# Performance work log

Hardware: AMD Instinct MI355X
Metric: run time of the kernel (lower is better)

The kernel has to match this reference:

```python
import jax, jax.numpy as jnp
import numpy as np

D_MODEL = 1024
N_HEADS = 16
DEPTH = D_MODEL // N_HEADS
B, S = 2, 2048


def setup_inputs() -> dict:
    key = jax.random.key(0)
    ks = jax.random.split(key, 11)
    scale = 1.0 / np.sqrt(D_MODEL)
    return {
        "q": jax.random.normal(ks[0], (B, S, D_MODEL), jnp.float32),
        "k": jax.random.normal(ks[1], (B, S, D_MODEL), jnp.float32),
        "v": jax.random.normal(ks[2], (B, S, D_MODEL), jnp.float32),
        "wq": jax.random.normal(ks[3], (D_MODEL, D_MODEL), jnp.float32) * scale,
        "bq": jnp.zeros((D_MODEL,), jnp.float32),
        "wk": jax.random.normal(ks[4], (D_MODEL, D_MODEL), jnp.float32) * scale,
        "bk": jnp.zeros((D_MODEL,), jnp.float32),
        "wv": jax.random.normal(ks[5], (D_MODEL, D_MODEL), jnp.float32) * scale,
        "bv": jnp.zeros((D_MODEL,), jnp.float32),
        "wo": jax.random.normal(ks[6], (D_MODEL, D_MODEL), jnp.float32) * scale,
        "bo": jnp.zeros((D_MODEL,), jnp.float32),
    }


def _mha(q, k, v, wq, bq, wk, bk, wv, bv, wo, bo):
    b, s, _ = q.shape
    # separate QKV projections
    qh = (q @ wq + bq).reshape(b, s, N_HEADS, DEPTH).transpose(0, 2, 1, 3)  # [b,h,s,d]
    kh = (k @ wk + bk).reshape(b, s, N_HEADS, DEPTH).transpose(0, 2, 1, 3)
    vh = (v @ wv + bv).reshape(b, s, N_HEADS, DEPTH).transpose(0, 2, 1, 3)
    # keras.layers.Attention default: UNSCALED dot-product scores, causal mask
    scores = jnp.einsum("bhqd,bhkd->bhqk", qh, kh)  # [b,h,s,s]
    causal = jnp.tril(jnp.ones((s, s), bool))
    scores = jnp.where(causal, scores, jnp.float32(-1e9))
    attn = jax.nn.softmax(scores, axis=-1)
    out = jnp.einsum("bhqk,bhkd->bhqd", attn, vh)  # [b,h,s,d]
    out = out.transpose(0, 2, 1, 3).reshape(b, s, D_MODEL)
    return out @ wo + bo


def reference(q, k, v, wq, bq, wk, bk, wv, bv, wo, bo):
    return _mha(q, k, v, wq, bq, wk, bk, wv, bv, wo, bo)
```

## Files before the change

kernel.cpp:

```cpp
#include <hip/hip_runtime.h>
#include <stdint.h>

#define AS1q __attribute__((address_space(1)))
#define AS3q __attribute__((address_space(3)))

typedef unsigned short US;
typedef __bf16 bf16x8 __attribute__((ext_vector_type(8)));
typedef float f32x4 __attribute__((ext_vector_type(4)));
typedef float f32x2 __attribute__((ext_vector_type(2)));
typedef __bf16 bf16x2 __attribute__((ext_vector_type(2)));

__device__ __forceinline__ US f2bf(float f) {
  union { float f; uint32_t u; } c; c.f = f;
  uint32_t u = c.u;
  return (US)((u + 0x7fffu + ((u >> 16) & 1u)) >> 16);
}

__device__ __forceinline__ bf16x8 asb(uint4 u) {
  union { uint4 u; bf16x8 b; } c; c.u = u; return c.b;
}

__device__ __forceinline__ void gload16(const void* g, void* l) {
  __builtin_amdgcn_global_load_lds((AS1q void*)(void*)g, (AS3q void*)l, 16, 0, 0);
}

__global__ void prep_kernel(const float* __restrict__ q, const float* __restrict__ k,
                            const float* __restrict__ v,
                            const float* __restrict__ w0, const float* __restrict__ w1,
                            const float* __restrict__ w2, const float* __restrict__ w3,
                            US* __restrict__ qb, US* __restrict__ kb, US* __restrict__ vb,
                            US* __restrict__ t0, US* __restrict__ t1,
                            US* __restrict__ t2, US* __restrict__ t3) {
  __shared__ US T[64 * 68];
  const int bx = blockIdx.x;
  const int t = threadIdx.x;
  if (bx < 6144) {
    const int ten = bx >> 11, chunk = bx & 2047;
    const float* s; US* d;
    if (ten == 0)      { s = q; d = qb; }
    else if (ten == 1) { s = k; d = kb; }
    else               { s = v; d = vb; }
    int i = (chunk * 256 + t) * 8;
    float4 f0 = *(const float4*)&s[i];
    float4 f1 = *(const float4*)&s[i + 4];
    ushort4 u0, u1;
    u0.x = f2bf(f0.x); u0.y = f2bf(f0.y); u0.z = f2bf(f0.z); u0.w = f2bf(f0.w);
    u1.x = f2bf(f1.x); u1.y = f2bf(f1.y); u1.z = f2bf(f1.z); u1.w = f2bf(f1.w);
    *(ushort4*)&d[i] = u0;
    *(ushort4*)&d[i + 4] = u1;
    return;
  }
  const int idx = bx - 6144;
  const int wsel = idx >> 8, rem = idx & 255;
  const int n0 = (rem & 15) * 64, k0 = (rem >> 4) * 64;
  const float* W; US* Wt;
  if (wsel == 0)      { W = w0; Wt = t0; }
  else if (wsel == 1) { W = w1; Wt = t1; }
  else if (wsel == 2) { W = w2; Wt = t2; }
  else                { W = w3; Wt = t3; }
#pragma unroll
  for (int it = 0; it < 4; ++it) {
    int p = t + it * 256;
    int row = p >> 4, c4 = (p & 15) * 4;
    float4 f = *(const float4*)&W[(k0 + row) * 1024 + n0 + c4];
    ushort4 u;
    u.x = f2bf(f.x); u.y = f2bf(f.y); u.z = f2bf(f.z); u.w = f2bf(f.w);
    *(ushort4*)&T[row * 68 + c4] = u;
  }
  __syncthreads();
#pragma unroll
  for (int it = 0; it < 4; ++it) {
    int p = t + it * 256;
    int rn = p >> 4, ck = (p & 15) * 4;
    ushort4 o;
    o.x = T[(ck + 0) * 68 + rn];
    o.y = T[(ck + 1) * 68 + rn];
    o.z = T[(ck + 2) * 68 + rn];
    o.w = T[(ck + 3) * 68 + rn];
    *(ushort4*)&Wt[(n0 + rn) * 1024 + k0 + ck] = o;
  }
}

template <bool SWAP>
__device__ __forceinline__ void gemm_core(const US* A, const US* Wt,
                                          int m0, int n0, US* As, US* Bs,
                                          f32x4 acc[4][4]) {
  const int tid = threadIdx.x;
  const int wave = tid >> 6, lane = tid & 63;
  const int quad = lane >> 4, l16 = lane & 15;
  const int wm = wave >> 1, wn = wave & 1;
#pragma unroll
  for (int i = 0; i < 4; ++i)
#pragma unroll
    for (int j = 0; j < 4; ++j) acc[i][j] = (f32x4)0.0f;
  const int p = wave * 64 + lane;
  const int arow0 = p >> 2, koff = (p & 3) * 8;
  for (int k0 = 0; k0 < 1024; k0 += 32) {
    gload16(A + (m0 + arow0) * 1024 + k0 + koff, As + wave * 512);
    gload16(A + (m0 + arow0 + 64) * 1024 + k0 + koff, As + 2048 + wave * 512);
    gload16(Wt + (n0 + arow0) * 1024 + k0 + koff, Bs + wave * 512);
    gload16(Wt + (n0 + arow0 + 64) * 1024 + k0 + koff, Bs + 2048 + wave * 512);
    __syncthreads();
    uint4 af[4], bf_[4];
#pragma unroll
    for (int mt = 0; mt < 4; ++mt)
      af[mt] = *(const uint4*)&As[(wm * 64 + mt * 16 + l16) * 32 + quad * 8];
#pragma unroll
    for (int nt = 0; nt < 4; ++nt)
      bf_[nt] = *(const uint4*)&Bs[(wn * 64 + nt * 16 + l16) * 32 + quad * 8];
#pragma unroll
    for (int i = 0; i < 4; ++i)
#pragma unroll
      for (int j = 0; j < 4; ++j) {
        if (SWAP)
          acc[i][j] = __builtin_amdgcn_mfma_f32_16x16x32_bf16(asb(bf_[i]), asb(af[j]),
                                                              acc[i][j], 0, 0, 0);
        else
          acc[i][j] = __builtin_amdgcn_mfma_f32_16x16x32_bf16(asb(af[i]), asb(bf_[j]),
                                                              acc[i][j], 0, 0, 0);
      }
    __syncthreads();
  }
}

__global__ __launch_bounds__(256, 4) void gemm_qkv_kernel(
    const US* __restrict__ qb, const US* __restrict__ kb, const US* __restrict__ vb,
    const US* __restrict__ wfT,
    const float* __restrict__ bq, const float* __restrict__ bk, const float* __restrict__ bv,
    US* __restrict__ qh, US* __restrict__ kh, US* __restrict__ vt) {
  __shared__ __align__(16) US As[4096], Bs[4096];
  const int m0 = blockIdx.x * 128, n0 = blockIdx.y * 128;
  const int which = n0 >> 10;
  const int nl0 = n0 & 1023;
  const US* A = (which == 0) ? qb : (which == 1) ? kb : vb;
  const float* bias = (which == 0) ? bq : (which == 1) ? bk : bv;
  const int tid = threadIdx.x, wave = tid >> 6, lane = tid & 63;
  const int quad = lane >> 4, l16 = lane & 15;
  const int wm = wave >> 1, wn = wave & 1;
  f32x4 acc[4][4];
  if (which == 2) {
    gemm_core<true>(A, wfT, m0, n0, As, Bs, acc);
#pragma unroll
    for (int nt = 0; nt < 4; ++nt) {
      int dg = nl0 + wn * 64 + nt * 16 + quad * 4;
#pragma unroll
      for (int r = 0; r < 4; ++r) {
        int d = dg + r;
        float bval = bias[d];
        int hh = d >> 6, dd = d & 63;
#pragma unroll
        for (int mt = 0; mt < 4; ++mt) {
          int sg = m0 + wm * 64 + mt * 16;
          int bb = sg >> 11, ss = sg & 2047;
          vt[(((size_t)bb * 16 + hh) * 64 + dd) * 2048 + ss + l16] =
              f2bf(acc[nt][mt][r] + bval);
        }
      }
    }
  } else {
    gemm_core<false>(A, wfT, m0, n0, As, Bs, acc);
    US* O = (which == 0) ? qh : kh;
#pragma unroll
    for (int nt = 0; nt < 4; ++nt) {
      int nl = nl0 + wn * 64 + nt * 16 + l16;
      float bval = bias[nl];
      int hh = nl >> 6, d = nl & 63;
#pragma unroll
      for (int mt = 0; mt < 4; ++mt) {
#pragma unroll
        for (int r = 0; r < 4; ++r) {
          int m = m0 + wm * 64 + mt * 16 + quad * 4 + r;
          int bb = m >> 11, s = m & 2047;
          O[((bb * 16 + hh) * 2048 + s) * 64 + d] = f2bf(acc[mt][nt][r] + bval);
        }
      }
    }
  }
}

__global__ __launch_bounds__(256, 4) void gemm_out_kernel(
    const US* __restrict__ ao, const US* __restrict__ woT,
    const float* __restrict__ bo, float* __restrict__ out) {
  __shared__ __align__(16) US As[4096], Bs[2048];
  const int m0 = blockIdx.x * 128, n0 = blockIdx.y * 64;
  const int tid = threadIdx.x;
  const int wave = tid >> 6, lane = tid & 63;
  const int quad = lane >> 4, l16 = lane & 15;
  f32x4 acc[2][4];
#pragma unroll
  for (int i = 0; i < 2; ++i)
#pragma unroll
    for (int j = 0; j < 4; ++j) acc[i][j] = (f32x4)0.0f;
  const int arow0 = tid >> 2, koff = (tid & 3) * 8;
  for (int k0 = 0; k0 < 1024; k0 += 32) {
    gload16(ao + (m0 + arow0) * 1024 + k0 + koff, As + wave * 512);
    gload16(ao + (m0 + arow0 + 64) * 1024 + k0 + koff, As + 2048 + wave * 512);
    gload16(woT + (n0 + arow0) * 1024 + k0 + koff, Bs + wave * 512);
    __syncthreads();
    uint4 af[2], bf_[4];
#pragma unroll
    for (int mt = 0; mt < 2; ++mt)
      af[mt] = *(const uint4*)&As[(wave * 32 + mt * 16 + l16) * 32 + quad * 8];
#pragma unroll
    for (int nt = 0; nt < 4; ++nt)
      bf_[nt] = *(const uint4*)&Bs[(nt * 16 + l16) * 32 + quad * 8];
#pragma unroll
    for (int mt = 0; mt < 2; ++mt)
#pragma unroll
      for (int nt = 0; nt < 4; ++nt)
        acc[mt][nt] = __builtin_amdgcn_mfma_f32_16x16x32_bf16(asb(af[mt]), asb(bf_[nt]),
                                                              acc[mt][nt], 0, 0, 0);
    __syncthreads();
  }
#pragma unroll
  for (int nt = 0; nt < 4; ++nt) {
    int n = n0 + nt * 16 + l16;
    float bval = bo[n];
#pragma unroll
    for (int mt = 0; mt < 2; ++mt) {
#pragma unroll
      for (int r = 0; r < 4; ++r) {
        int m = m0 + wave * 32 + mt * 16 + quad * 4 + r;
        out[m * 1024 + n] = acc[mt][nt][r] + bval;
      }
    }
  }
}

__global__ __launch_bounds__(512, 6) void attn_kernel(
    const US* __restrict__ qh, const US* __restrict__ kh,
    const US* __restrict__ vt, US* __restrict__ aout) {
  __shared__ __align__(16) US Ks[2][4096];
  __shared__ __align__(16) US Vs[2][4096];
  __shared__ __align__(16) union UU {
    struct { US Qs[4096]; US Ps[8 * 640]; } s;
    struct { float Oex[4][16][65]; float lEx[4][16]; } e;
  } u;
  const int tid = threadIdx.x;
  const int wave = tid >> 6, lane = tid & 63;
  const int quad = lane >> 4, l16 = lane & 15;
  const int w_m = wave & 3, w_k = wave >> 2;
  const int bh = blockIdx.x;
  const int b = bh >> 4, h = bh & 15;
  const int g = blockIdx.y;

  int t0, t1;
  if (g < 11)      { t0 = 31 - g; t1 = -1; }
  else if (g < 19) { int j = g - 11; t0 = 16 - j; t1 = j; }
  else if (g < 23) { t0 = 17 + (g - 19); t1 = -1; }
  else             { t0 = 8; t1 = -1; }

  const int srow = tid >> 3, sc = (tid & 7) ^ (srow & 7);
  const US* gkb = kh + (size_t)bh * 2048 * 64;
  const US* gvb = vt + (size_t)bh * 64 * 2048;

  for (int ei = 0; ei < 2; ++ei) {
    const int qt = ei ? t1 : t0;
    if (qt < 0) break;
    const int q0 = qt * 64;
    __syncthreads();
    {
      const US* gq = qh + ((size_t)bh * 2048 + q0) * 64;
      gload16(gq + srow * 64 + sc * 8, u.s.Qs + wave * 512);
      gload16(gkb + srow * 64 + sc * 8, Ks[0] + wave * 512);
      gload16(gvb + srow * 2048 + sc * 8, Vs[0] + wave * 512);
    }
    __syncthreads();

    const int qrow = w_m * 16 + l16;
    uint4 aq0 = *(const uint4*)&u.s.Qs[qrow * 64 + ((quad ^ (qrow & 7)) * 8)];
    uint4 aq1 = *(const uint4*)&u.s.Qs[qrow * 64 + (((4 + quad) ^ (qrow & 7)) * 8)];

    float l_part[4] = {0.f, 0.f, 0.f, 0.f};
    f32x4 Of[4];
#pragma unroll
    for (int nt = 0; nt < 4; ++nt) Of[nt] = (f32x4)0.0f;
    const int grow_base = q0 + w_m * 16 + quad * 4;

    US* pw = u.s.Ps + wave * 640;

    for (int kt = 0; kt <= qt; ++kt) {
      const int cb = kt & 1;
      if (kt) __syncthreads();
      if (kt < qt) {
        const US* gk = gkb + (kt + 1) * 64 * 64;
        const US* gv = gvb + (kt + 1) * 64;
        gload16(gk + srow * 64 + sc * 8, Ks[cb ^ 1] + wave * 512);
        gload16(gv + srow * 2048 + sc * 8, Vs[cb ^ 1] + wave * 512);
      }
      const US* Kc = Ks[cb];
      const US* Vc = Vs[cb];

      f32x4 sacc[2];
      sacc[0] = (f32x4)0.0f; sacc[1] = (f32x4)0.0f;
#pragma unroll
      for (int nt = 0; nt < 2; ++nt) {
        int krow = w_k * 32 + nt * 16 + l16;
        uint4 bk0 = *(const uint4*)&Kc[krow * 64 + ((quad ^ (krow & 7)) * 8)];
        sacc[nt] = __builtin_amdgcn_mfma_f32_16x16x32_bf16(asb(aq0), asb(bk0), sacc[nt], 0, 0, 0);
      }
#pragma unroll
      for (int nt = 0; nt < 2; ++nt) {
        int krow = w_k * 32 + nt * 16 + l16;
        uint4 bk1 = *(const uint4*)&Kc[krow * 64 + (((4 + quad) ^ (krow & 7)) * 8)];
        sacc[nt] = __builtin_amdgcn_mfma_f32_16x16x32_bf16(asb(aq1), asb(bk1), sacc[nt], 0, 0, 0);
      }
      if (kt == qt) {
#pragma unroll
        for (int nt = 0; nt < 2; ++nt) {
          int gcol = q0 + w_k * 32 + nt * 16 + l16;
#pragma unroll
          for (int r = 0; r < 4; ++r)
            if (gcol > grow_base + r) sacc[nt][r] = -1e30f;
        }
      }

#pragma unroll
      for (int nt = 0; nt < 2; ++nt) {
#pragma unroll
        for (int r = 0; r < 4; r += 2) {
          float e0 = __expf(sacc[nt][r]);
          float e1 = __expf(sacc[nt][r + 1]);
          l_part[r] += e0;
          l_part[r + 1] += e1;
          f32x2 fv; fv[0] = e0; fv[1] = e1;
          bf16x2 bv2 = __builtin_convertvector(fv, bf16x2);
          union { bf16x2 b; ushort2 u; } cc; cc.b = bv2;
          pw[(quad * 4 + r) * 40 + nt * 16 + l16] = cc.u.x;
          pw[(quad * 4 + r + 1) * 40 + nt * 16 + l16] = cc.u.y;
        }
      }
      __asm__ volatile("s_waitcnt lgkmcnt(0)" ::: "memory");

      uint4 ap = *(const uint4*)&pw[l16 * 40 + quad * 8];
#pragma unroll
      for (int nt = 0; nt < 4; ++nt) {
        int vrow = nt * 16 + l16;
        uint4 bv_ = *(const uint4*)&Vc[vrow * 64 + (((w_k * 4 + quad) ^ (vrow & 7)) * 8)];
        Of[nt] = __builtin_amdgcn_mfma_f32_16x16x32_bf16(asb(ap), asb(bv_), Of[nt], 0, 0, 0);
      }
    }

    float l_red[4];
#pragma unroll
    for (int r = 0; r < 4; ++r) {
      float s = l_part[r];
#pragma unroll
      for (int off = 1; off < 16; off <<= 1) s += __shfl_xor(s, off, 64);
      l_red[r] = s;
    }

    __syncthreads();
    if (w_k == 1) {
#pragma unroll
      for (int nt = 0; nt < 4; ++nt)
#pragma unroll
        for (int r = 0; r < 4; ++r)
          u.e.Oex[w_m][quad * 4 + r][nt * 16 + l16] = Of[nt][r];
      if (l16 == 0) {
#pragma unroll
        for (int r = 0; r < 4; ++r) u.e.lEx[w_m][quad * 4 + r] = l_red[r];
      }
    }
    __syncthreads();
    if (w_k == 0) {
#pragma unroll
      for (int r = 0; r < 4; ++r) {
        float ltot = l_red[r] + u.e.lEx[w_m][quad * 4 + r];
        float inv = 1.0f / ltot;
        int row = grow_base + r;
#pragma unroll
        for (int nt = 0; nt < 4; ++nt) {
          float o = Of[nt][r] + u.e.Oex[w_m][quad * 4 + r][nt * 16 + l16];
          aout[((size_t)b * 2048 + row) * 1024 + h * 64 + nt * 16 + l16] = f2bf(o * inv);
        }
      }
    }
  }
}

extern "C" void kernel_launch(void* const* d_in, const int* in_sizes, int n_in,
                              void* d_out, int out_size, void* d_ws, size_t ws_size,
                              hipStream_t stream) {
  const float* q  = (const float*)d_in[0];
  const float* k  = (const float*)d_in[1];
  const float* v  = (const float*)d_in[2];
  const float* wq = (const float*)d_in[3];
  const float* bq = (const float*)d_in[4];
  const float* wk = (const float*)d_in[5];
  const float* bk = (const float*)d_in[6];
  const float* wv = (const float*)d_in[7];
  const float* bv = (const float*)d_in[8];
  const float* wo = (const float*)d_in[9];
  const float* bo = (const float*)d_in[10];
  float* out = (float*)d_out;

  char* ws = (char*)d_ws;
  const size_t MB = 1024 * 1024;
  US* qb  = (US*)(ws + 0 * MB);
  US* kb  = (US*)(ws + 8 * MB);
  US* vb  = (US*)(ws + 16 * MB);
  US* wqT = (US*)(ws + 24 * MB);
  US* wkT = (US*)(ws + 26 * MB);
  US* wvT = (US*)(ws + 28 * MB);
  US* woT = (US*)(ws + 30 * MB);
  US* qh  = (US*)(ws + 32 * MB);
  US* kh  = (US*)(ws + 40 * MB);
  US* vt  = (US*)(ws + 48 * MB);
  US* ao  = (US*)(ws + 56 * MB);

  prep_kernel<<<7168, 256, 0, stream>>>(q, k, v, wq, wk, wv, wo,
                                        qb, kb, vb, wqT, wkT, wvT, woT);
  gemm_qkv_kernel<<<dim3(32, 24), 256, 0, stream>>>(qb, kb, vb, wqT,
                                                    bq, bk, bv, qh, kh, vt);
  attn_kernel<<<dim3(32, 24), 512, 0, stream>>>(qh, kh, vt, ao);
  gemm_out_kernel<<<dim3(32, 16), 256, 0, stream>>>(ao, woT, bo, out);
}
```

Measured before the change: 208.6 us.

## Use 32x32x16 MFMA in attention with 4 waves and exp2-prescaled Q

The attention kernel moves from 8 waves using 16x16x32 MFMA tiles to 4 waves per block using 32x32x16 MFMA tiles. Each wave now owns a 32x32 score tile, which cuts LDS fragment reloads per flop and the number of MFMA issues. Q is prescaled by log2(e) in the QKV projection epilogue so the softmax can call the native exp2 in place of __expf. The trade-offs are half as many waves per block, more registers per wave, and wider cross-lane reductions of the row sums.

```diff
diff --git a/kernel.cpp b/kernel.cpp
--- a/kernel.cpp
+++ b/kernel.cpp
@@ -7,8 +7,11 @@
 typedef unsigned short US;
 typedef __bf16 bf16x8 __attribute__((ext_vector_type(8)));
 typedef float f32x4 __attribute__((ext_vector_type(4)));
+typedef float f32x16 __attribute__((ext_vector_type(16)));
 typedef float f32x2 __attribute__((ext_vector_type(2)));
 typedef __bf16 bf16x2 __attribute__((ext_vector_type(2)));
+
+#define LOG2E 1.44269504088896340736f
 
 __device__ __forceinline__ US f2bf(float f) {
   union { float f; uint32_t u; } c; c.f = f;
@@ -160,6 +163,7 @@
   } else {
     gemm_core<false>(A, wfT, m0, n0, As, Bs, acc);
     US* O = (which == 0) ? qh : kh;
+    const float scale = (which == 0) ? LOG2E : 1.0f;
 #pragma unroll
     for (int nt = 0; nt < 4; ++nt) {
       int nl = nl0 + wn * 64 + nt * 16 + l16;
@@ -171,7 +175,7 @@
         for (int r = 0; r < 4; ++r) {
           int m = m0 + wm * 64 + mt * 16 + quad * 4 + r;
           int bb = m >> 11, s = m & 2047;
-          O[((bb * 16 + hh) * 2048 + s) * 64 + d] = f2bf(acc[mt][nt][r] + bval);
+          O[((bb * 16 + hh) * 2048 + s) * 64 + d] = f2bf((acc[mt][nt][r] + bval) * scale);
         }
       }
     }
@@ -227,19 +231,19 @@
   }
 }
 
-__global__ __launch_bounds__(512, 6) void attn_kernel(
+__global__ __launch_bounds__(256, 3) void attn_kernel(
     const US* __restrict__ qh, const US* __restrict__ kh,
     const US* __restrict__ vt, US* __restrict__ aout) {
   __shared__ __align__(16) US Ks[2][4096];
   __shared__ __align__(16) US Vs[2][4096];
   __shared__ __align__(16) union UU {
-    struct { US Qs[4096]; US Ps[8 * 640]; } s;
-    struct { float Oex[4][16][65]; float lEx[4][16]; } e;
+    struct { US Qs[4096]; US Ps[4][1280]; } s;
+    struct { float Oex[64][65]; float lEx[64]; } e;
   } u;
   const int tid = threadIdx.x;
   const int wave = tid >> 6, lane = tid & 63;
-  const int quad = lane >> 4, l16 = lane & 15;
-  const int w_m = wave & 3, w_k = wave >> 2;
+  const int l31 = lane & 31, lh = lane >> 5;
+  const int w_m = wave & 1, w_k = wave >> 1;
   const int bh = blockIdx.x;
   const int b = bh >> 4, h = bh & 15;
   const int g = blockIdx.y;
@@ -250,7 +254,10 @@
   else if (g < 23) { t0 = 17 + (g - 19); t1 = -1; }
   else             { t0 = 8; t1 = -1; }
 
-  const int srow = tid >> 3, sc = (tid & 7) ^ (srow & 7);
+  const int p1 = tid, p2 = tid + 256;
+  const int row1 = p1 >> 3, c1 = (p1 & 7) ^ (row1 & 7);
+  const int row2 = p2 >> 3, c2 = (p2 & 7) ^ (row2 & 7);
+
   const US* gkb = kh + (size_t)bh * 2048 * 64;
   const US* gvb = vt + (size_t)bh * 64 * 2048;
 
@@ -261,23 +268,28 @@
     __syncthreads();
     {
       const US* gq = qh + ((size_t)bh * 2048 + q0) * 64;
-      gload16(gq + srow * 64 + sc * 8, u.s.Qs + wave * 512);
-      gload16(gkb + srow * 64 + sc * 8, Ks[0] + wave * 512);
-      gload16(gvb + srow * 2048 + sc * 8, Vs[0] + wave * 512);
-    }
-    __syncthreads();
-
-    const int qrow = w_m * 16 + l16;
-    uint4 aq0 = *(const uint4*)&u.s.Qs[qrow * 64 + ((quad ^ (qrow & 7)) * 8)];
-    uint4 aq1 = *(const uint4*)&u.s.Qs[qrow * 64 + (((4 + quad) ^ (qrow & 7)) * 8)];
-
-    float l_part[4] = {0.f, 0.f, 0.f, 0.f};
-    f32x4 Of[4];
-#pragma unroll
-    for (int nt = 0; nt < 4; ++nt) Of[nt] = (f32x4)0.0f;
-    const int grow_base = q0 + w_m * 16 + quad * 4;
-
-    US* pw = u.s.Ps + wave * 640;
+      gload16(gq + row1 * 64 + c1 * 8, u.s.Qs + wave * 512);
+      gload16(gq + row2 * 64 + c2 * 8, u.s.Qs + 2048 + wave * 512);
+      gload16(gkb + row1 * 64 + c1 * 8, Ks[0] + wave * 512);
+      gload16(gkb + row2 * 64 + c2 * 8, Ks[0] + 2048 + wave * 512);
+      gload16(gvb + row1 * 2048 + c1 * 8, Vs[0] + wave * 512);
+      gload16(gvb + row2 * 2048 + c2 * 8, Vs[0] + 2048 + wave * 512);
+    }
+    __syncthreads();
+
+    const int ql = w_m * 32 + l31;
+    uint4 aq[4];
+#pragma unroll
+    for (int dc = 0; dc < 4; ++dc)
+      aq[dc] = *(const uint4*)&u.s.Qs[ql * 64 + (((dc * 2 + lh) ^ (ql & 7)) * 8)];
+
+    float l_part[16];
+#pragma unroll
+    for (int r = 0; r < 16; ++r) l_part[r] = 0.0f;
+    f32x16 Of0 = (f32x16)0.0f, Of1 = (f32x16)0.0f;
+
+    US* pw = u.s.Ps[wave];
+    const int kl = w_k * 32 + l31;
 
     for (int kt = 0; kt <= qt; ++kt) {
       const int cb = kt & 1;
@@ -285,95 +297,92 @@
       if (kt < qt) {
         const US* gk = gkb + (kt + 1) * 64 * 64;
         const US* gv = gvb + (kt + 1) * 64;
-        gload16(gk + srow * 64 + sc * 8, Ks[cb ^ 1] + wave * 512);
-        gload16(gv + srow * 2048 + sc * 8, Vs[cb ^ 1] + wave * 512);
+        gload16(gk + row1 * 64 + c1 * 8, Ks[cb ^ 1] + wave * 512);
+        gload16(gk + row2 * 64 + c2 * 8, Ks[cb ^ 1] + 2048 + wave * 512);
+        gload16(gv + row1 * 2048 + c1 * 8, Vs[cb ^ 1] + wave * 512);
+        gload16(gv + row2 * 2048 + c2 * 8, Vs[cb ^ 1] + 2048 + wave * 512);
       }
       const US* Kc = Ks[cb];
       const US* Vc = Vs[cb];
 
-      f32x4 sacc[2];
-      sacc[0] = (f32x4)0.0f; sacc[1] = (f32x4)0.0f;
-#pragma unroll
-      for (int nt = 0; nt < 2; ++nt) {
-        int krow = w_k * 32 + nt * 16 + l16;
-        uint4 bk0 = *(const uint4*)&Kc[krow * 64 + ((quad ^ (krow & 7)) * 8)];
-        sacc[nt] = __builtin_amdgcn_mfma_f32_16x16x32_bf16(asb(aq0), asb(bk0), sacc[nt], 0, 0, 0);
-      }
-#pragma unroll
-      for (int nt = 0; nt < 2; ++nt) {
-        int krow = w_k * 32 + nt * 16 + l16;
-        uint4 bk1 = *(const uint4*)&Kc[krow * 64 + (((4 + quad) ^ (krow & 7)) * 8)];
-        sacc[nt] = __builtin_amdgcn_mfma_f32_16x16x32_bf16(asb(aq1), asb(bk1), sacc[nt], 0, 0, 0);
+      f32x16 sacc = (f32x16)0.0f;
+#pragma unroll
+      for (int dc = 0; dc < 4; ++dc) {
+        uint4 kb_ = *(const uint4*)&Kc[kl * 64 + (((dc * 2 + lh) ^ (kl & 7)) * 8)];
+        sacc = __builtin_amdgcn_mfma_f32_32x32x16_bf16(asb(aq[dc]), asb(kb_), sacc, 0, 0, 0);
       }
       if (kt == qt) {
-#pragma unroll
-        for (int nt = 0; nt < 2; ++nt) {
-          int gcol = q0 + w_k * 32 + nt * 16 + l16;
-#pragma unroll
-          for (int r = 0; r < 4; ++r)
-            if (gcol > grow_base + r) sacc[nt][r] = -1e30f;
+        int gcol = q0 + w_k * 32 + l31;
+#pragma unroll
+        for (int r = 0; r < 16; ++r) {
+          int grow = q0 + w_m * 32 + 4 * lh + 8 * (r >> 2) + (r & 3);
+          if (gcol > grow) sacc[r] = -1e30f;
         }
       }
 
 #pragma unroll
-      for (int nt = 0; nt < 2; ++nt) {
-#pragma unroll
-        for (int r = 0; r < 4; r += 2) {
-          float e0 = __expf(sacc[nt][r]);
-          float e1 = __expf(sacc[nt][r + 1]);
-          l_part[r] += e0;
-          l_part[r + 1] += e1;
-          f32x2 fv; fv[0] = e0; fv[1] = e1;
-          bf16x2 bv2 = __builtin_convertvector(fv, bf16x2);
-          union { bf16x2 b; ushort2 u; } cc; cc.b = bv2;
-          pw[(quad * 4 + r) * 40 + nt * 16 + l16] = cc.u.x;
-          pw[(quad * 4 + r + 1) * 40 + nt * 16 + l16] = cc.u.y;
+      for (int r = 0; r < 16; r += 2) {
+        float e0 = __builtin_amdgcn_exp2f(sacc[r]);
+        float e1 = __builtin_amdgcn_exp2f(sacc[r + 1]);
+        l_part[r] += e0;
+        l_part[r + 1] += e1;
+        f32x2 fv; fv[0] = e0; fv[1] = e1;
+        bf16x2 bv2 = __builtin_convertvector(fv, bf16x2);
+        union { bf16x2 b; ushort2 u; } cc; cc.b = bv2;
+        int row0 = 4 * lh + 8 * (r >> 2) + (r & 3);
+        pw[row0 * 40 + l31] = cc.u.x;
+        pw[(row0 + 1) * 40 + l31] = cc.u.y;
+      }
+      __asm__ volatile("s_waitcnt lgkmcnt(0)" ::: "memory");
+
+      uint4 ap0 = *(const uint4*)&pw[l31 * 40 + lh * 8];
+      uint4 ap1 = *(const uint4*)&pw[l31 * 40 + 16 + lh * 8];
+#pragma unroll
+      for (int dh = 0; dh < 2; ++dh) {
+        int vrow = dh * 32 + l31;
+        uint4 bv0 = *(const uint4*)&Vc[vrow * 64 + (((w_k * 4 + lh) ^ (vrow & 7)) * 8)];
+        uint4 bv1 = *(const uint4*)&Vc[vrow * 64 + (((w_k * 4 + 2 + lh) ^ (vrow & 7)) * 8)];
+        if (dh == 0) {
+          Of0 = __builtin_amdgcn_mfma_f32_32x32x16_bf16(asb(ap0), asb(bv0), Of0, 0, 0, 0);
+          Of0 = __builtin_amdgcn_mfma_f32_32x32x16_bf16(asb(ap1), asb(bv1), Of0, 0, 0, 0);
+        } else {
+          Of1 = __builtin_amdgcn_mfma_f32_32x32x16_bf16(asb(ap0), asb(bv0), Of1, 0, 0, 0);
+          Of1 = __builtin_amdgcn_mfma_f32_32x32x16_bf16(asb(ap1), asb(bv1), Of1, 0, 0, 0);
         }
       }
-      __asm__ volatile("s_waitcnt lgkmcnt(0)" ::: "memory");
-
-      uint4 ap = *(const uint4*)&pw[l16 * 40 + quad * 8];
-#pragma unroll
-      for (int nt = 0; nt < 4; ++nt) {
-        int vrow = nt * 16 + l16;
-        uint4 bv_ = *(const uint4*)&Vc[vrow * 64 + (((w_k * 4 + quad) ^ (vrow & 7)) * 8)];
-        Of[nt] = __builtin_amdgcn_mfma_f32_16x16x32_bf16(asb(ap), asb(bv_), Of[nt], 0, 0, 0);
-      }
-    }
-
-    float l_red[4];
-#pragma unroll
-    for (int r = 0; r < 4; ++r) {
-      float s = l_part[r];
-#pragma unroll
-      for (int off = 1; off < 16; off <<= 1) s += __shfl_xor(s, off, 64);
-      l_red[r] = s;
+    }
+
+#pragma unroll
+    for (int r = 0; r < 16; ++r) {
+#pragma unroll
+      for (int off = 1; off < 32; off <<= 1)
+        l_part[r] += __shfl_xor(l_part[r], off, 64);
     }
 
     __syncthreads();
     if (w_k == 1) {
 #pragma unroll
-      for (int nt = 0; nt < 4; ++nt)
-#pragma unroll
-        for (int r = 0; r < 4; ++r)
-          u.e.Oex[w_m][quad * 4 + r][nt * 16 + l16] = Of[nt][r];
-      if (l16 == 0) {
-#pragma unroll
-        for (int r = 0; r < 4; ++r) u.e.lEx[w_m][quad * 4 + r] = l_red[r];
+      for (int r = 0; r < 16; ++r) {
+        int row = w_m * 32 + 4 * lh + 8 * (r >> 2) + (r & 3);
+        u.e.Oex[row][l31] = Of0[r];
+        u.e.Oex[row][32 + l31] = Of1[r];
+        if (l31 == 0) u.e.lEx[row] = l_part[r];
       }
     }
     __syncthreads();
     if (w_k == 0) {
 #pragma unroll
-      for (int r = 0; r < 4; ++r) {
-        float ltot = l_red[r] + u.e.lEx[w_m][quad * 4 + r];
+      for (int r = 0; r < 16; ++r) {
+        int rl = 4 * lh + 8 * (r >> 2) + (r & 3);
+        int row = w_m * 32 + rl;
+        float ltot = l_part[r] + u.e.lEx[row];
         float inv = 1.0f / ltot;
-        int row = grow_base + r;
-#pragma unroll
-        for (int nt = 0; nt < 4; ++nt) {
-          float o = Of[nt][r] + u.e.Oex[w_m][quad * 4 + r][nt * 16 + l16];
-          aout[((size_t)b * 2048 + row) * 1024 + h * 64 + nt * 16 + l16] = f2bf(o * inv);
-        }
+        int grow = q0 + row;
+        float o0 = Of0[r] + u.e.Oex[row][l31];
+        float o1 = Of1[r] + u.e.Oex[row][32 + l31];
+        US* dst = aout + ((size_t)b * 2048 + grow) * 1024 + h * 64;
+        dst[l31] = f2bf(o0 * inv);
+        dst[32 + l31] = f2bf(o1 * inv);
       }
     }
   }
@@ -413,6 +422,6 @@
                                         qb, kb, vb, wqT, wkT, wvT, woT);
   gemm_qkv_kernel<<<dim3(32, 24), 256, 0, stream>>>(qb, kb, vb, wqT,
                                                     bq, bk, bv, qh, kh, vt);
-  attn_kernel<<<dim3(32, 24), 512, 0, stream>>>(qh, kh, vt, ao);
+  attn_kernel<<<dim3(32, 24), 256, 0, stream>>>(qh, kh, vt, ao);
   gemm_out_kernel<<<dim3(32, 16), 256, 0, stream>>>(ao, woT, bo, out);
 }
```

Result: no change. 208.9 us (+0.2%).

## Restructure causal attention around 32x32 MFMA, 128-key tiles and register-resident P

Applied to the files above, without the earlier changes.

Rewrites the attention kernel to use 256-thread blocks with 32x32x16 bf16 MFMAs over 128-key tiles. It computes S transposed so the exp'd probabilities are repacked into MFMA operands through cross-lane shuffles instead of a round trip through LDS. log2(e) is folded into the Q projection epilogue so softmax uses the native exp2. Each block handles a balanced pair of query tiles (qt, 31-qt) on a 32x16 grid, and the final normalization writes 16-byte vector stores. The cost is more LDS per block (72 KB) and lower occupancy, and the 128-key diagonal tile wastes some masked work.

```diff
diff --git a/kernel.cpp b/kernel.cpp
--- a/kernel.cpp
+++ b/kernel.cpp
@@ -7,8 +7,11 @@
 typedef unsigned short US;
 typedef __bf16 bf16x8 __attribute__((ext_vector_type(8)));
 typedef float f32x4 __attribute__((ext_vector_type(4)));
+typedef float f32x16 __attribute__((ext_vector_type(16)));
 typedef float f32x2 __attribute__((ext_vector_type(2)));
 typedef __bf16 bf16x2 __attribute__((ext_vector_type(2)));
+
+#define LOG2E 1.44269504088896340736f
 
 __device__ __forceinline__ US f2bf(float f) {
   union { float f; uint32_t u; } c; c.f = f;
@@ -18,6 +21,12 @@
 
 __device__ __forceinline__ bf16x8 asb(uint4 u) {
   union { uint4 u; bf16x8 b; } c; c.u = u; return c.b;
+}
+
+__device__ __forceinline__ uint32_t pk2(float a, float b) {
+  f32x2 fv; fv[0] = a; fv[1] = b;
+  bf16x2 bb = __builtin_convertvector(fv, bf16x2);
+  union { bf16x2 b; uint32_t u; } c; c.b = bb; return c.u;
 }
 
 __device__ __forceinline__ void gload16(const void* g, void* l) {
@@ -160,6 +169,7 @@
   } else {
     gemm_core<false>(A, wfT, m0, n0, As, Bs, acc);
     US* O = (which == 0) ? qh : kh;
+    const float scale = (which == 0) ? LOG2E : 1.0f;
 #pragma unroll
     for (int nt = 0; nt < 4; ++nt) {
       int nl = nl0 + wn * 64 + nt * 16 + l16;
@@ -171,7 +181,7 @@
         for (int r = 0; r < 4; ++r) {
           int m = m0 + wm * 64 + mt * 16 + quad * 4 + r;
           int bb = m >> 11, s = m & 2047;
-          O[((bb * 16 + hh) * 2048 + s) * 64 + d] = f2bf(acc[mt][nt][r] + bval);
+          O[((bb * 16 + hh) * 2048 + s) * 64 + d] = f2bf((acc[mt][nt][r] + bval) * scale);
         }
       }
     }
@@ -227,154 +237,178 @@
   }
 }
 
-__global__ __launch_bounds__(512, 6) void attn_kernel(
+__global__ __launch_bounds__(256, 2) void attn_kernel(
     const US* __restrict__ qh, const US* __restrict__ kh,
     const US* __restrict__ vt, US* __restrict__ aout) {
-  __shared__ __align__(16) US Ks[2][4096];
-  __shared__ __align__(16) US Vs[2][4096];
-  __shared__ __align__(16) union UU {
-    struct { US Qs[4096]; US Ps[8 * 640]; } s;
-    struct { float Oex[4][16][65]; float lEx[4][16]; } e;
-  } u;
+  __shared__ __align__(16) char arena[73728];
+  US* KsA = (US*)arena;
+  US* VsA = (US*)(arena + 32768);
+  US* Qs  = (US*)(arena + 65536);
+  float* Oex = (float*)arena;
+  float* lEx = (float*)(arena + 34816);
+
   const int tid = threadIdx.x;
   const int wave = tid >> 6, lane = tid & 63;
-  const int quad = lane >> 4, l16 = lane & 15;
-  const int w_m = wave & 3, w_k = wave >> 2;
+  const int l31 = lane & 31, lh = lane >> 5;
+  const int w_m = wave & 1, w_k = wave >> 1;
   const int bh = blockIdx.x;
   const int b = bh >> 4, h = bh & 15;
-  const int g = blockIdx.y;
-
-  int t0, t1;
-  if (g < 11)      { t0 = 31 - g; t1 = -1; }
-  else if (g < 19) { int j = g - 11; t0 = 16 - j; t1 = j; }
-  else if (g < 23) { t0 = 17 + (g - 19); t1 = -1; }
-  else             { t0 = 8; t1 = -1; }
-
-  const int srow = tid >> 3, sc = (tid & 7) ^ (srow & 7);
+  const int jg = blockIdx.y;
+
   const US* gkb = kh + (size_t)bh * 2048 * 64;
   const US* gvb = vt + (size_t)bh * 64 * 2048;
 
   for (int ei = 0; ei < 2; ++ei) {
-    const int qt = ei ? t1 : t0;
-    if (qt < 0) break;
+    const int qt = ei ? jg : (31 - jg);
     const int q0 = qt * 64;
+    const int nit = (qt >> 1) + 1;
     __syncthreads();
     {
       const US* gq = qh + ((size_t)bh * 2048 + q0) * 64;
-      gload16(gq + srow * 64 + sc * 8, u.s.Qs + wave * 512);
-      gload16(gkb + srow * 64 + sc * 8, Ks[0] + wave * 512);
-      gload16(gvb + srow * 2048 + sc * 8, Vs[0] + wave * 512);
-    }
-    __syncthreads();
-
-    const int qrow = w_m * 16 + l16;
-    uint4 aq0 = *(const uint4*)&u.s.Qs[qrow * 64 + ((quad ^ (qrow & 7)) * 8)];
-    uint4 aq1 = *(const uint4*)&u.s.Qs[qrow * 64 + (((4 + quad) ^ (qrow & 7)) * 8)];
-
-    float l_part[4] = {0.f, 0.f, 0.f, 0.f};
-    f32x4 Of[4];
-#pragma unroll
-    for (int nt = 0; nt < 4; ++nt) Of[nt] = (f32x4)0.0f;
-    const int grow_base = q0 + w_m * 16 + quad * 4;
-
-    US* pw = u.s.Ps + wave * 640;
-
-    for (int kt = 0; kt <= qt; ++kt) {
-      const int cb = kt & 1;
-      if (kt) __syncthreads();
-      if (kt < qt) {
-        const US* gk = gkb + (kt + 1) * 64 * 64;
-        const US* gv = gvb + (kt + 1) * 64;
-        gload16(gk + srow * 64 + sc * 8, Ks[cb ^ 1] + wave * 512);
-        gload16(gv + srow * 2048 + sc * 8, Vs[cb ^ 1] + wave * 512);
-      }
-      const US* Kc = Ks[cb];
-      const US* Vc = Vs[cb];
-
-      f32x4 sacc[2];
-      sacc[0] = (f32x4)0.0f; sacc[1] = (f32x4)0.0f;
-#pragma unroll
-      for (int nt = 0; nt < 2; ++nt) {
-        int krow = w_k * 32 + nt * 16 + l16;
-        uint4 bk0 = *(const uint4*)&Kc[krow * 64 + ((quad ^ (krow & 7)) * 8)];
-        sacc[nt] = __builtin_amdgcn_mfma_f32_16x16x32_bf16(asb(aq0), asb(bk0), sacc[nt], 0, 0, 0);
-      }
-#pragma unroll
-      for (int nt = 0; nt < 2; ++nt) {
-        int krow = w_k * 32 + nt * 16 + l16;
-        uint4 bk1 = *(const uint4*)&Kc[krow * 64 + (((4 + quad) ^ (krow & 7)) * 8)];
-        sacc[nt] = __builtin_amdgcn_mfma_f32_16x16x32_bf16(asb(aq1), asb(bk1), sacc[nt], 0, 0, 0);
-      }
-      if (kt == qt) {
-#pragma unroll
-        for (int nt = 0; nt < 2; ++nt) {
-          int gcol = q0 + w_k * 32 + nt * 16 + l16;
-#pragma unroll
-          for (int r = 0; r < 4; ++r)
-            if (gcol > grow_base + r) sacc[nt][r] = -1e30f;
-        }
-      }
-
-#pragma unroll
-      for (int nt = 0; nt < 2; ++nt) {
-#pragma unroll
-        for (int r = 0; r < 4; r += 2) {
-          float e0 = __expf(sacc[nt][r]);
-          float e1 = __expf(sacc[nt][r + 1]);
-          l_part[r] += e0;
-          l_part[r + 1] += e1;
-          f32x2 fv; fv[0] = e0; fv[1] = e1;
-          bf16x2 bv2 = __builtin_convertvector(fv, bf16x2);
-          union { bf16x2 b; ushort2 u; } cc; cc.b = bv2;
-          pw[(quad * 4 + r) * 40 + nt * 16 + l16] = cc.u.x;
-          pw[(quad * 4 + r + 1) * 40 + nt * 16 + l16] = cc.u.y;
-        }
-      }
-      __asm__ volatile("s_waitcnt lgkmcnt(0)" ::: "memory");
-
-      uint4 ap = *(const uint4*)&pw[l16 * 40 + quad * 8];
-#pragma unroll
-      for (int nt = 0; nt < 4; ++nt) {
-        int vrow = nt * 16 + l16;
-        uint4 bv_ = *(const uint4*)&Vc[vrow * 64 + (((w_k * 4 + quad) ^ (vrow & 7)) * 8)];
-        Of[nt] = __builtin_amdgcn_mfma_f32_16x16x32_bf16(asb(ap), asb(bv_), Of[nt], 0, 0, 0);
-      }
-    }
-
-    float l_red[4];
-#pragma unroll
-    for (int r = 0; r < 4; ++r) {
-      float s = l_part[r];
-#pragma unroll
-      for (int off = 1; off < 16; off <<= 1) s += __shfl_xor(s, off, 64);
-      l_red[r] = s;
-    }
-
-    __syncthreads();
-    if (w_k == 1) {
-#pragma unroll
-      for (int nt = 0; nt < 4; ++nt)
-#pragma unroll
-        for (int r = 0; r < 4; ++r)
-          u.e.Oex[w_m][quad * 4 + r][nt * 16 + l16] = Of[nt][r];
-      if (l16 == 0) {
-#pragma unroll
-        for (int r = 0; r < 4; ++r) u.e.lEx[w_m][quad * 4 + r] = l_red[r];
-      }
-    }
-    __syncthreads();
-    if (w_k == 0) {
-#pragma unroll
-      for (int r = 0; r < 4; ++r) {
-        float ltot = l_red[r] + u.e.lEx[w_m][quad * 4 + r];
-        float inv = 1.0f / ltot;
-        int row = grow_base + r;
-#pragma unroll
-        for (int nt = 0; nt < 4; ++nt) {
-          float o = Of[nt][r] + u.e.Oex[w_m][quad * 4 + r][nt * 16 + l16];
-          aout[((size_t)b * 2048 + row) * 1024 + h * 64 + nt * 16 + l16] = f2bf(o * inv);
-        }
-      }
+#pragma unroll
+      for (int ro = 0; ro < 2; ++ro) {
+        int p = tid + ro * 256;
+        int row = p >> 3, c = (p & 7) ^ (row & 7);
+        gload16(gq + row * 64 + c * 8, Qs + ro * 2048 + wave * 512);
+      }
+#pragma unroll
+      for (int ro = 0; ro < 4; ++ro) {
+        int p = tid + ro * 256;
+        int row = p >> 3, c = (p & 7) ^ (row & 7);
+        gload16(gkb + row * 64 + c * 8, KsA + ro * 2048 + wave * 512);
+      }
+#pragma unroll
+      for (int ro = 0; ro < 4; ++ro) {
+        int p = tid + ro * 256;
+        int row = p >> 4, c = (p & 15) ^ (row & 15);
+        gload16(gvb + row * 2048 + c * 8, VsA + ro * 2048 + wave * 512);
+      }
+    }
+    __syncthreads();
+
+    const int qrow = w_m * 32 + l31;
+    uint4 bq[4];
+#pragma unroll
+    for (int s = 0; s < 4; ++s)
+      bq[s] = *(const uint4*)&Qs[qrow * 64 + (((2 * s + lh) ^ (qrow & 7)) * 8)];
+    const int q_g = q0 + qrow;
+
+    float l_lane = 0.0f;
+    f32x16 Oa0 = (f32x16)0.0f, Oa1 = (f32x16)0.0f;
+
+    for (int it = 0; it < nit; ++it) {
+      const int cb = it & 1;
+      const int kb = it * 128;
+      if (it) __syncthreads();
+      if (it + 1 < nit) {
+        const US* gk = gkb + (kb + 128) * 64;
+        const US* gv = gvb + (kb + 128);
+        US* kd = KsA + (cb ^ 1) * 8192;
+        US* vd = VsA + (cb ^ 1) * 8192;
+#pragma unroll
+        for (int ro = 0; ro < 4; ++ro) {
+          int p = tid + ro * 256;
+          int row = p >> 3, c = (p & 7) ^ (row & 7);
+          gload16(gk + row * 64 + c * 8, kd + ro * 2048 + wave * 512);
+        }
+#pragma unroll
+        for (int ro = 0; ro < 4; ++ro) {
+          int p = tid + ro * 256;
+          int row = p >> 4, c = (p & 15) ^ (row & 15);
+          gload16(gv + row * 2048 + c * 8, vd + ro * 2048 + wave * 512);
+        }
+      }
+      const US* Kc = KsA + cb * 8192;
+      const US* Vc = VsA + cb * 8192;
+
+      f32x16 sa0 = (f32x16)0.0f, sa1 = (f32x16)0.0f;
+#pragma unroll
+      for (int s = 0; s < 4; ++s) {
+        int kr0 = w_k * 64 + l31;
+        uint4 ka0 = *(const uint4*)&Kc[kr0 * 64 + (((2 * s + lh) ^ (kr0 & 7)) * 8)];
+        sa0 = __builtin_amdgcn_mfma_f32_32x32x16_bf16(asb(ka0), asb(bq[s]), sa0, 0, 0, 0);
+      }
+#pragma unroll
+      for (int s = 0; s < 4; ++s) {
+        int kr1 = w_k * 64 + 32 + l31;
+        uint4 ka1 = *(const uint4*)&Kc[kr1 * 64 + (((2 * s + lh) ^ (kr1 & 7)) * 8)];
+        sa1 = __builtin_amdgcn_mfma_f32_32x32x16_bf16(asb(ka1), asb(bq[s]), sa1, 0, 0, 0);
+      }
+
+      const bool diag = (it == nit - 1);
+      float e[2][16];
+#pragma unroll
+      for (int ta = 0; ta < 2; ++ta) {
+        const int kbase = kb + w_k * 64 + ta * 32 + 4 * lh;
+#pragma unroll
+        for (int r = 0; r < 16; ++r) {
+          float sv = ta ? sa1[r] : sa0[r];
+          float ev = __builtin_amdgcn_exp2f(sv);
+          if (diag) {
+            int key_g = kbase + (r & 3) + 8 * (r >> 2);
+            if (key_g > q_g) ev = 0.0f;
+          }
+          e[ta][r] = ev;
+          l_lane += ev;
+        }
+      }
+
+#pragma unroll
+      for (int ta = 0; ta < 2; ++ta) {
+#pragma unroll
+        for (int s2 = 0; s2 < 2; ++s2) {
+          uint32_t PA0 = pk2(e[ta][8 * s2 + 0], e[ta][8 * s2 + 1]);
+          uint32_t PA1 = pk2(e[ta][8 * s2 + 2], e[ta][8 * s2 + 3]);
+          uint32_t PB0 = pk2(e[ta][8 * s2 + 4], e[ta][8 * s2 + 5]);
+          uint32_t PB1 = pk2(e[ta][8 * s2 + 6], e[ta][8 * s2 + 7]);
+          uint32_t XA0 = (uint32_t)__shfl_xor((int)PA0, 32, 64);
+          uint32_t XA1 = (uint32_t)__shfl_xor((int)PA1, 32, 64);
+          uint32_t XB0 = (uint32_t)__shfl_xor((int)PB0, 32, 64);
+          uint32_t XB1 = (uint32_t)__shfl_xor((int)PB1, 32, 64);
+          uint4 bp;
+          bp.x = lh ? XB0 : PA0;
+          bp.y = lh ? XB1 : PA1;
+          bp.z = lh ? PB0 : XA0;
+          bp.w = lh ? PB1 : XA1;
+          const int c_log = w_k * 8 + ta * 4 + s2 * 2 + lh;
+          int vr0 = l31;
+          uint4 va0 = *(const uint4*)&Vc[vr0 * 128 + ((c_log ^ (vr0 & 15)) * 8)];
+          Oa0 = __builtin_amdgcn_mfma_f32_32x32x16_bf16(asb(va0), asb(bp), Oa0, 0, 0, 0);
+          int vr1 = 32 + l31;
+          uint4 va1 = *(const uint4*)&Vc[vr1 * 128 + ((c_log ^ (vr1 & 15)) * 8)];
+          Oa1 = __builtin_amdgcn_mfma_f32_32x32x16_bf16(asb(va1), asb(bp), Oa1, 0, 0, 0);
+        }
+      }
+    }
+
+    float l_q = l_lane + __shfl_xor(l_lane, 32, 64);
+
+    __syncthreads();
+    {
+      float* myO = Oex + w_k * (64 * 68);
+      int q_idx = w_m * 32 + l31;
+#pragma unroll
+      for (int r = 0; r < 16; ++r) {
+        int dr = 4 * lh + (r & 3) + 8 * (r >> 2);
+        myO[q_idx * 68 + dr] = Oa0[r];
+        myO[q_idx * 68 + 32 + dr] = Oa1[r];
+      }
+      if (lh == 0) lEx[w_k * 64 + q_idx] = l_q;
+    }
+    __syncthreads();
+    {
+      int q_idx = tid >> 2;
+      int dseg = (tid & 3) * 16;
+      float inv = 1.0f / (lEx[q_idx] + lEx[64 + q_idx]);
+      union { US s[16]; uint4 v[2]; } ob;
+#pragma unroll
+      for (int t2 = 0; t2 < 16; ++t2) {
+        float o = Oex[q_idx * 68 + dseg + t2] + Oex[64 * 68 + q_idx * 68 + dseg + t2];
+        ob.s[t2] = f2bf(o * inv);
+      }
+      US* dst = aout + ((size_t)b * 2048 + q0 + q_idx) * 1024 + h * 64 + dseg;
+      *(uint4*)dst = ob.v[0];
+      *(uint4*)(dst + 8) = ob.v[1];
     }
   }
 }
@@ -413,6 +447,6 @@
                                         qb, kb, vb, wqT, wkT, wvT, woT);
   gemm_qkv_kernel<<<dim3(32, 24), 256, 0, stream>>>(qb, kb, vb, wqT,
                                                     bq, bk, bv, qh, kh, vt);
-  attn_kernel<<<dim3(32, 24), 512, 0, stream>>>(qh, kh, vt, ao);
+  attn_kernel<<<dim3(32, 16), 256, 0, stream>>>(qh, kh, vt, ao);
   gemm_out_kernel<<<dim3(32, 16), 256, 0, stream>>>(ao, woT, bo, out);
 }
```

Result: no change. 208.0 us (-0.3%).
